# Performance work log

Hardware: AMD Instinct MI355X
Metric: run time of the kernel (lower is better)

## Reference

```python
import jax, jax.numpy as jnp
import numpy as np

D_MODEL = 1024
D_RES = 1024
EPS = 1e-5


def setup_inputs() -> dict:
    key = jax.random.key(0)
    ks = jax.random.split(key, 8)
    S, B = 2048, 32
    scale_ih = 1.0 / np.sqrt(D_MODEL)
    x = jax.random.normal(ks[0], (S, B, D_RES), dtype=jnp.float32)
    # nn.RNN params: weight_ih_l0 [H, I], weight_hh_l0 [H, H], biases [H]
    W_ih = jax.random.uniform(ks[1], (D_MODEL, D_RES), jnp.float32, -scale_ih, scale_ih)
    W_hh = jax.random.uniform(ks[2], (D_MODEL, D_MODEL), jnp.float32, -scale_ih, scale_ih)
    b_ih = jax.random.uniform(ks[3], (D_MODEL,), jnp.float32, -scale_ih, scale_ih)
    b_hh = jax.random.uniform(ks[4], (D_MODEL,), jnp.float32, -scale_ih, scale_ih)
    # out_proj: Linear(d_model, d_res, bias=False) -> weight [d_res, d_model]
    W_out = jax.random.uniform(ks[5], (D_RES, D_MODEL), jnp.float32, -scale_ih, scale_ih)
    ln_g = jnp.ones((D_RES,), jnp.float32)
    ln_b = jnp.zeros((D_RES,), jnp.float32)
    return {"x": x, "W_ih": W_ih, "W_hh": W_hh, "b_ih": b_ih, "b_hh": b_hh,
            "W_out": W_out, "ln_g": ln_g, "ln_b": ln_b}


def _layer_norm(x, g, b):
    mu = jnp.mean(x, axis=-1, keepdims=True)
    var = jnp.mean(jnp.square(x - mu), axis=-1, keepdims=True)
    return (x - mu) * jax.lax.rsqrt(var + EPS) * g + b


def _rnn_tanh(x, W_ih, W_hh, b_ih, b_hh):
    # x: [S, B, I]; precompute input projection once (one big GEMM)
    pre = jnp.einsum('sbi,hi->sbh', x, W_ih) + b_ih + b_hh  # [S, B, H]
    B = x.shape[1]
    h0 = jnp.zeros((B, W_hh.shape[0]), x.dtype)

    def step(h, p_t):
        h_new = jnp.tanh(p_t + h @ W_hh.T)
        return h_new, h_new

    _, hs = jax.lax.scan(step, h0, pre)  # hs: [S, B, H]
    return hs


def reference(x, W_ih, W_hh, b_ih, b_hh, W_out, ln_g, ln_b):
    # pre_lnorm=False, use_out_proj=True, use_res=True, use_lnorm=True, dropout=0 (eval)
    attn_out = _rnn_tanh(x, W_ih, W_hh, b_ih, b_hh)          # [S, B, d_model]
    attn_out = jnp.einsum('sbh,rh->sbr', attn_out, W_out)    # [S, B, d_res]
    return _layer_norm(x + attn_out, ln_g, ln_b)
```

## Files before the change

### kernel.cpp

```cpp
#include <hip/hip_runtime.h>
#include <hip/hip_bf16.h>

typedef __bf16 bf16x8 __attribute__((ext_vector_type(8)));
typedef __bf16 bf16x4 __attribute__((ext_vector_type(4)));
typedef float  f32x4  __attribute__((ext_vector_type(4)));
typedef unsigned int u32x2 __attribute__((ext_vector_type(2)));
typedef unsigned int u32x4 __attribute__((ext_vector_type(4)));

#define NSTEP 2048
#define NB    32
#define DH    1024
#define MTOT  (NSTEP * NB)
#define NWORK 16
#define NFILL 208
#define FILLER_CAP 60000

__device__ __forceinline__ f32x4 mfma16(bf16x8 a, bf16x8 b, f32x4 c) {
    return __builtin_amdgcn_mfma_f32_16x16x32_bf16(a, b, c, 0, 0, 0);
}

__device__ __forceinline__ void load_lds16(const __bf16* g, void* l) {
    __builtin_amdgcn_global_load_lds(
        (const __attribute__((address_space(1))) void*)g,
        (__attribute__((address_space(3))) void*)l, 16, 0, 0);
}

__device__ __forceinline__ float tanh_fast(float x) {
    float e = exp2f(x * 2.8853900817779268f);
    return 1.0f - 2.0f * __builtin_amdgcn_rcpf(e + 1.0f);
}

__global__ __launch_bounds__(256) void prep_kernel(
    const float* __restrict__ Wih, const float* __restrict__ Whh,
    const float* __restrict__ Wout, const float* __restrict__ bih,
    const float* __restrict__ bhh,
    __bf16* __restrict__ Wih_b, __bf16* __restrict__ Whh_b,
    __bf16* __restrict__ Wout_b, float* __restrict__ bias,
    int* __restrict__ flags)
{
    const int i = blockIdx.x * 256 + threadIdx.x;
    const size_t off = (size_t)i * 4;
    {
        float4 a = *(const float4*)(Wih + off);
        bf16x4 o = {(__bf16)a.x, (__bf16)a.y, (__bf16)a.z, (__bf16)a.w};
        *(bf16x4*)(Wih_b + off) = o;
    }
    {
        float4 a = *(const float4*)(Whh + off);
        bf16x4 o = {(__bf16)a.x, (__bf16)a.y, (__bf16)a.z, (__bf16)a.w};
        *(bf16x4*)(Whh_b + off) = o;
    }
    {
        float4 a = *(const float4*)(Wout + off);
        bf16x4 o = {(__bf16)a.x, (__bf16)a.y, (__bf16)a.z, (__bf16)a.w};
        *(bf16x4*)(Wout_b + off) = o;
    }
    if (i < DH) bias[i] = bih[i] + bhh[i];
    if (i < 64) {
        int z = 0;
        asm volatile("global_store_dword %0, %1, off sc0 sc1"
                     :: "v"(&flags[i]), "v"(z) : "memory");
    }
}

__global__ __launch_bounds__(256) void cvt_bf16_x(
    const float* __restrict__ in, __bf16* __restrict__ outb)
{
    const size_t i = ((size_t)blockIdx.x * 256 + threadIdx.x) * 8;
    float4 a = *(const float4*)(in + i);
    float4 b = *(const float4*)(in + i + 4);
    bf16x8 o = { (__bf16)a.x, (__bf16)a.y, (__bf16)a.z, (__bf16)a.w,
                 (__bf16)b.x, (__bf16)b.y, (__bf16)b.z, (__bf16)b.w };
    *(bf16x8*)(outb + i) = o;
}

__global__ __launch_bounds__(256) void gemm_bt(
    const __bf16* __restrict__ A,
    const __bf16* __restrict__ B,
    const float*  __restrict__ bias,
    __bf16* __restrict__ C,
    int M, int N, int K)
{
    __shared__ __bf16 sA[128 * 64];
    __shared__ __bf16 sB[128 * 64];
    const int nTn = N >> 7;
    const int tm = (int)(blockIdx.x / nTn) << 7;
    const int tn = (int)(blockIdx.x % nTn) << 7;
    const int t = threadIdx.x;
    const int w = t >> 6, l = t & 63;
    const int wy = w & 1, wx = w >> 1;
    const int l16 = l & 15, lhi = l >> 4;
    const int rw = t >> 3;
    const int kc = (t & 7) << 3;

    const __bf16* ga = A + (size_t)(tm + rw) * K + kc;
    const __bf16* gb = B + (size_t)(tn + rw) * K + kc;
    char* lA = (char*)sA + (w * 8) * 128;
    char* lB = (char*)sB + (w * 8) * 128;

    f32x4 acc[4][4] = {};

    for (int k0 = 0; k0 < K; k0 += 64) {
#pragma unroll
        for (int i = 0; i < 4; ++i) {
            load_lds16(ga + (size_t)(i * 32) * K + k0, lA + i * 32 * 128);
            load_lds16(gb + (size_t)(i * 32) * K + k0, lB + i * 32 * 128);
        }
        asm volatile("s_waitcnt vmcnt(0)" ::: "memory");
        __syncthreads();
#pragma unroll
        for (int kk = 0; kk < 2; ++kk) {
            bf16x8 af[4], bfr[4];
#pragma unroll
            for (int i = 0; i < 4; ++i) {
                af[i]  = *(const bf16x8*)(sA + (wy * 64 + i * 16 + l16) * 64 + kk * 32 + lhi * 8);
                bfr[i] = *(const bf16x8*)(sB + (wx * 64 + i * 16 + l16) * 64 + kk * 32 + lhi * 8);
            }
#pragma unroll
            for (int i = 0; i < 4; ++i)
#pragma unroll
                for (int j = 0; j < 4; ++j)
                    acc[i][j] = mfma16(af[i], bfr[j], acc[i][j]);
        }
        __syncthreads();
    }
#pragma unroll
    for (int j = 0; j < 4; ++j) {
        const int col = tn + wx * 64 + j * 16 + l16;
        const float bv = bias ? bias[col] : 0.0f;
#pragma unroll
        for (int i = 0; i < 4; ++i) {
            __bf16* cp = C + (size_t)(tm + wy * 64 + i * 16 + lhi * 4) * N + col;
#pragma unroll
            for (int r = 0; r < 4; ++r)
                cp[(size_t)r * N] = (__bf16)(acc[i][j][r] + bv);
        }
    }
}

#define LDU(d, p) asm volatile("global_load_dwordx4 %0, %1, off sc0 sc1" \
                               : "=v"(d) : "v"(p) : "memory");

__global__ __launch_bounds__(512, 2) void rnn_scan(
    const __bf16* __restrict__ Whh,
    const __bf16* __restrict__ pre,
    __bf16* __restrict__ hs,
    __bf16* __restrict__ hx,
    int* __restrict__ flags)
{
    const int gb = blockIdx.x;
    if (gb >= NWORK) {
        float a = (float)(threadIdx.x + gb) * 1.0e-6f + 1.0f;
        const float m = 1.000001f, d = 0.999999f;
        const int* dp = flags;
        for (int it = 0; it < FILLER_CAP; ++it) {
#pragma unroll
            for (int u = 0; u < 128; ++u) {
                a = __builtin_fmaf(a, m, 1.0e-12f);
                a = __builtin_fmaf(a, d, -1.0e-12f);
            }
            if ((it & 15) == 0) {
                int dn;
                asm volatile("global_load_dword %0, %1, off sc0 sc1\n\t"
                             "s_waitcnt vmcnt(0)"
                             : "=v"(dn) : "v"(dp) : "memory");
                if (dn != 0) break;
            }
        }
        asm volatile("" :: "v"(a));
        return;
    }

    __shared__ char slab[2][65536];
    const int t = threadIdx.x;
    const int w = t >> 6;
    const int l = t & 63;
    const int mhalf = w & 1;
    const int jg = w >> 1;
    const int j0 = gb * 64 + jg * 16;
    const int l16 = l & 15;
    const int lhi = l >> 4;
    const int b  = mhalf * 16 + l16;
    const int jc = j0 + lhi * 4;

    bf16x8 wreg[32];
    {
        const __bf16* wb = Whh + (size_t)(j0 + l16) * DH + lhi * 8;
#pragma unroll
        for (int c = 0; c < 32; ++c)
            wreg[c] = *(const bf16x8*)(wb + c * 32);
    }

    const unsigned rbase = (unsigned)b * 2048 + (unsigned)lhi * 16;
    const unsigned rx = (unsigned)((b & 7) << 4);

    for (int s = 0; s < NSTEP; ++s) {
        bf16x4 pv = *(const bf16x4*)(pre + ((size_t)s * NB + b) * DH + jc);

        f32x4 acc0 = {0.f, 0.f, 0.f, 0.f}, acc1 = acc0, acc2 = acc0, acc3 = acc0;
        int bi = 0;

        if (s > 0) {
            const int sl = s - 1;
            bi = sl & 1;
            const unsigned rep = (unsigned)(((sl >> 1) & 1) + 1) * 0x00010001u;
            const char* sp = (const char*)hx + ((size_t)(sl & 1) << 16) + (size_t)t * 16;
            const char* p0 = sp;
            const char* p1 = sp + 8192;
            const char* p2 = sp + 16384;
            const char* p3 = sp + 24576;
            const char* p4 = sp + 32768;
            const char* p5 = sp + 40960;
            const char* p6 = sp + 49152;
            const char* p7 = sp + 57344;
            u32x4 st[8];
            for (;;) {
                LDU(st[0], p0) LDU(st[1], p1) LDU(st[2], p2) LDU(st[3], p3)
                LDU(st[4], p4) LDU(st[5], p5) LDU(st[6], p6) LDU(st[7], p7)
                asm volatile("s_waitcnt vmcnt(0)" ::: "memory");
                __builtin_amdgcn_sched_barrier(0);
                unsigned bad = 0;
#pragma unroll
                for (int i = 0; i < 8; ++i)
                    bad |= (st[i][0] ^ rep) | (st[i][1] ^ rep)
                         | (st[i][2] ^ rep) | (st[i][3] ^ rep);
                if (__all((bad & 0x00030003u) == 0u)) break;
            }
            __builtin_amdgcn_sched_barrier(0);
#pragma unroll
            for (int i = 0; i < 8; ++i) {
                unsigned byte = (unsigned)t * 16 + (unsigned)i * 8192;
                unsigned row = byte >> 11;
                unsigned swz = byte ^ ((row & 7) << 4);
                *(u32x4*)(&slab[bi][swz]) = st[i];
            }
            __syncthreads();
#pragma unroll
            for (int c = 0; c < 32; c += 4) {
                bf16x8 h0 = *(const bf16x8*)(&slab[bi][(rbase + (unsigned)(c + 0) * 64) ^ rx]);
                bf16x8 h1 = *(const bf16x8*)(&slab[bi][(rbase + (unsigned)(c + 1) * 64) ^ rx]);
                bf16x8 h2 = *(const bf16x8*)(&slab[bi][(rbase + (unsigned)(c + 2) * 64) ^ rx]);
                bf16x8 h3 = *(const bf16x8*)(&slab[bi][(rbase + (unsigned)(c + 3) * 64) ^ rx]);
                acc0 = mfma16(wreg[c + 0], h0, acc0);
                acc1 = mfma16(wreg[c + 1], h1, acc1);
                acc2 = mfma16(wreg[c + 2], h2, acc2);
                acc3 = mfma16(wreg[c + 3], h3, acc3);
            }
        }
        f32x4 accs = (acc0 + acc1) + (acc2 + acc3);

        float h0 = tanh_fast(accs[0] + (float)pv[0]);
        float h1 = tanh_fast(accs[1] + (float)pv[1]);
        float h2 = tanh_fast(accs[2] + (float)pv[2]);
        float h3 = tanh_fast(accs[3] + (float)pv[3]);
        const unsigned tag = (unsigned)(((s >> 1) & 1) + 1);
        unsigned u0 = (unsigned)__builtin_bit_cast(unsigned short, (__bf16)h0);
        unsigned u1 = (unsigned)__builtin_bit_cast(unsigned short, (__bf16)h1);
        unsigned u2 = (unsigned)__builtin_bit_cast(unsigned short, (__bf16)h2);
        unsigned u3 = (unsigned)__builtin_bit_cast(unsigned short, (__bf16)h3);
        u0 = ((u0 + 2u) & 0xFFFCu) | tag;
        u1 = ((u1 + 2u) & 0xFFFCu) | tag;
        u2 = ((u2 + 2u) & 0xFFFCu) | tag;
        u3 = ((u3 + 2u) & 0xFFFCu) | tag;
        u32x2 uval;
        uval[0] = u0 | (u1 << 16);
        uval[1] = u2 | (u3 << 16);
        __bf16* ox = hx + ((size_t)(s & 1) * NB + b) * DH + jc;
        asm volatile("global_store_dwordx2 %0, %1, off sc0 sc1"
                     :: "v"(ox), "v"(uval) : "memory");
        *(u32x2*)(hs + ((size_t)s * NB + b) * DH + jc) = uval;
    }
    if (gb == 0 && t == 0) {
        int one = 1;
        asm volatile("global_store_dword %0, %1, off sc0 sc1"
                     :: "v"(&flags[0]), "v"(one) : "memory");
    }
}

__global__ __launch_bounds__(256) void fused_ln(
    const float* __restrict__ x,
    const __bf16* __restrict__ attn,
    const float* __restrict__ gam,
    const float* __restrict__ bet,
    float* __restrict__ out)
{
    const int row = blockIdx.x;
    const int t = threadIdx.x;
    const size_t base = (size_t)row * DH + t * 4;
    float4 xv = *(const float4*)(x + base);
    bf16x4 av = *(const bf16x4*)(attn + base);
    float v0 = xv.x + (float)av[0];
    float v1 = xv.y + (float)av[1];
    float v2 = xv.z + (float)av[2];
    float v3 = xv.w + (float)av[3];
    float s1 = v0 + v1 + v2 + v3;
    float s2 = v0 * v0 + v1 * v1 + v2 * v2 + v3 * v3;
#pragma unroll
    for (int off = 32; off > 0; off >>= 1) {
        s1 += __shfl_xor(s1, off);
        s2 += __shfl_xor(s2, off);
    }
    __shared__ float red[8];
    const int w = t >> 6, l = t & 63;
    if (l == 0) { red[w] = s1; red[4 + w] = s2; }
    __syncthreads();
    float S1 = red[0] + red[1] + red[2] + red[3];
    float S2 = red[4] + red[5] + red[6] + red[7];
    const float mu = S1 * (1.0f / 1024.0f);
    const float var = S2 * (1.0f / 1024.0f) - mu * mu;
    const float rs = rsqrtf(var + 1e-5f);
    const int c = t * 4;
    float4 gv = *(const float4*)(gam + c);
    float4 bv = *(const float4*)(bet + c);
    float4 o;
    o.x = (v0 - mu) * rs * gv.x + bv.x;
    o.y = (v1 - mu) * rs * gv.y + bv.y;
    o.z = (v2 - mu) * rs * gv.z + bv.z;
    o.w = (v3 - mu) * rs * gv.w + bv.w;
    *(float4*)(out + base) = o;
}

extern "C" void kernel_launch(void* const* d_in, const int* in_sizes, int n_in,
                              void* d_out, int out_size, void* d_ws, size_t ws_size,
                              hipStream_t stream)
{
    const float* x    = (const float*)d_in[0];
    const float* Wih  = (const float*)d_in[1];
    const float* Whh  = (const float*)d_in[2];
    const float* bih  = (const float*)d_in[3];
    const float* bhh  = (const float*)d_in[4];
    const float* Wout = (const float*)d_in[5];
    const float* lng  = (const float*)d_in[6];
    const float* lnb  = (const float*)d_in[7];
    float* out = (float*)d_out;

    char* ws = (char*)d_ws;
    const size_t BIG = (size_t)MTOT * DH * sizeof(__bf16);
    __bf16* buf0   = (__bf16*)ws;
    __bf16* pre    = (__bf16*)(ws + BIG);
    __bf16* hsbuf  = (__bf16*)(ws + 2 * BIG);
    __bf16* Wih_b  = (__bf16*)(ws + 3 * BIG);
    __bf16* Whh_b  = Wih_b + (size_t)DH * DH;
    __bf16* Wout_b = Whh_b + (size_t)DH * DH;
    float*  bias   = (float*)(Wout_b + (size_t)DH * DH);
    int*    flags  = (int*)(bias + DH);
    __bf16* hx     = (__bf16*)(ws + 3 * BIG + 8 * 1024 * 1024);

    prep_kernel<<<1024, 256, 0, stream>>>(Wih, Whh, Wout, bih, bhh,
                                          Wih_b, Whh_b, Wout_b, bias, flags);
    cvt_bf16_x<<<32768, 256, 0, stream>>>(x, buf0);
    hipMemsetAsync(hx, 0, 2 * NB * DH * sizeof(__bf16), stream);
    gemm_bt<<<4096, 256, 0, stream>>>(buf0, Wih_b, bias, pre, MTOT, DH, DH);
    rnn_scan<<<NWORK + NFILL, 512, 0, stream>>>(Whh_b, pre, hsbuf, hx, flags);
    gemm_bt<<<4096, 256, 0, stream>>>(hsbuf, Wout_b, nullptr, buf0, MTOT, DH, DH);
    fused_ln<<<65536, 256, 0, stream>>>(x, buf0, lng, lnb, out);
}
```

Baseline: 8.397 ms.

## Split batch into four independent groups and pipeline RNN scan across sub-slots

Splits the 32-wide batch into four independent 8-row groups that are processed round-robin. While one group's hidden state is being published, the next group's state and pre-activations are prefetched, so the cross-block spin-wait latency is hidden behind other groups' work. Each of 8 worker blocks now owns 128 hidden columns instead of 16 blocks owning 64, with smaller LDS slabs and more filler blocks. The trade-off is that half of each MFMA tile is wasted on the 8-row batch (only half the lanes store results) and the number of sequential synchronisation rounds is four times larger.

```diff
diff --git a/kernel.cpp b/kernel.cpp
--- a/kernel.cpp
+++ b/kernel.cpp
@@ -11,9 +11,10 @@
 #define NB    32
 #define DH    1024
 #define MTOT  (NSTEP * NB)
-#define NWORK 16
-#define NFILL 208
-#define FILLER_CAP 60000
+#define NWORK 8
+#define NFILL 240
+#define FILLER_CAP 120000
+#define TMAX  (4 * NSTEP)
 
 __device__ __forceinline__ f32x4 mfma16(bf16x8 a, bf16x8 b, f32x4 c) {
     return __builtin_amdgcn_mfma_f32_16x16x32_bf16(a, b, c, 0, 0, 0);
@@ -138,10 +139,112 @@
     }
 }
 
-#define LDU(d, p) asm volatile("global_load_dwordx4 %0, %1, off sc0 sc1" \
-                               : "=v"(d) : "v"(p) : "memory");
-
-__global__ __launch_bounds__(512, 2) void rnn_scan(
+__device__ __forceinline__ void subslot(
+    int tau, int gb, int t, int bl, int jc, bool wlane,
+    unsigned wb0, unsigned wb1, unsigned rbase, unsigned rx,
+    const bf16x8* wreg,
+    const __bf16* __restrict__ pre,
+    __bf16* __restrict__ hs,
+    __bf16* __restrict__ hx,
+    char (&slab)[2][16384],
+    u32x4& pf0, u32x4& pf1, u32x2& pvn,
+    u32x2& uv, __bf16*& px, __bf16*& ps)
+{
+    const int p_ = tau & 3;
+    const int s_ = tau >> 2;
+    const int b_ = p_ * 8 + bl;
+    const int bi = tau & 1;
+    f32x4 a0 = {0.f, 0.f, 0.f, 0.f}, a1 = a0, a2 = a0, a3 = a0;
+    bf16x4 pv;
+
+    if (s_ > 0) {
+        asm volatile("s_waitcnt vmcnt(2)" ::: "memory");
+        __builtin_amdgcn_sched_barrier(0);
+        pv = __builtin_bit_cast(bf16x4, pvn);
+        const unsigned rep = (unsigned)((((s_ - 1) >> 1) & 1) + 1) * 0x00010001u;
+        const char* pb = (const char*)hx
+            + ((size_t)((p_ << 1) + ((s_ - 1) & 1)) << 14) + (size_t)t * 32;
+        for (;;) {
+            unsigned bad = (pf0[0] ^ rep) | (pf0[1] ^ rep) | (pf0[2] ^ rep) | (pf0[3] ^ rep)
+                         | (pf1[0] ^ rep) | (pf1[1] ^ rep) | (pf1[2] ^ rep) | (pf1[3] ^ rep);
+            if (__all((bad & 0x00030003u) == 0u)) break;
+            asm volatile("global_load_dwordx4 %0, %2, off sc0 sc1\n\t"
+                         "global_load_dwordx4 %1, %2, off offset:16 sc0 sc1\n\t"
+                         "s_waitcnt vmcnt(0)"
+                         : "=v"(pf0), "=v"(pf1) : "v"(pb) : "memory");
+            __builtin_amdgcn_sched_barrier(0);
+        }
+        *(u32x4*)(&slab[bi][wb0]) = pf0;
+        *(u32x4*)(&slab[bi][wb1]) = pf1;
+    } else {
+        asm volatile("global_load_dwordx2 %0, %1, off\n\t"
+                     "s_waitcnt vmcnt(0)"
+                     : "=v"(pvn)
+                     : "v"(pre + ((size_t)s_ * NB + b_) * DH + jc) : "memory");
+        __builtin_amdgcn_sched_barrier(0);
+        pv = __builtin_bit_cast(bf16x4, pvn);
+    }
+    __syncthreads();
+
+    {
+        const int t1 = tau + 1;
+        if (t1 < TMAX) {
+            const int p1 = t1 & 3, s1 = t1 >> 2;
+            if (s1 >= 1) {
+                const char* nb = (const char*)hx
+                    + ((size_t)((p1 << 1) + ((s1 - 1) & 1)) << 14) + (size_t)t * 32;
+                asm volatile("global_load_dwordx4 %0, %2, off sc0 sc1\n\t"
+                             "global_load_dwordx4 %1, %2, off offset:16 sc0 sc1"
+                             : "=v"(pf0), "=v"(pf1) : "v"(nb) : "memory");
+                asm volatile("global_load_dwordx2 %0, %1, off"
+                             : "=v"(pvn)
+                             : "v"(pre + ((size_t)s1 * NB + (p1 * 8 + bl)) * DH + jc)
+                             : "memory");
+            }
+        }
+    }
+
+    if (s_ > 0) {
+#pragma unroll
+        for (int c = 0; c < 32; c += 4) {
+            bf16x8 h0 = *(const bf16x8*)(&slab[bi][(rbase + (unsigned)(c + 0) * 64) ^ rx]);
+            bf16x8 h1 = *(const bf16x8*)(&slab[bi][(rbase + (unsigned)(c + 1) * 64) ^ rx]);
+            bf16x8 h2 = *(const bf16x8*)(&slab[bi][(rbase + (unsigned)(c + 2) * 64) ^ rx]);
+            bf16x8 h3 = *(const bf16x8*)(&slab[bi][(rbase + (unsigned)(c + 3) * 64) ^ rx]);
+            a0 = mfma16(wreg[c + 0], h0, a0);
+            a1 = mfma16(wreg[c + 1], h1, a1);
+            a2 = mfma16(wreg[c + 2], h2, a2);
+            a3 = mfma16(wreg[c + 3], h3, a3);
+        }
+    }
+    f32x4 as = (a0 + a1) + (a2 + a3);
+
+    float h0 = tanh_fast(as[0] + (float)pv[0]);
+    float h1 = tanh_fast(as[1] + (float)pv[1]);
+    float h2 = tanh_fast(as[2] + (float)pv[2]);
+    float h3 = tanh_fast(as[3] + (float)pv[3]);
+    const unsigned tag = (unsigned)(((s_ >> 1) & 1) + 1);
+    unsigned u0 = (unsigned)__builtin_bit_cast(unsigned short, (__bf16)h0);
+    unsigned u1 = (unsigned)__builtin_bit_cast(unsigned short, (__bf16)h1);
+    unsigned u2 = (unsigned)__builtin_bit_cast(unsigned short, (__bf16)h2);
+    unsigned u3 = (unsigned)__builtin_bit_cast(unsigned short, (__bf16)h3);
+    u0 = ((u0 + 2u) & 0xFFFCu) | tag;
+    u1 = ((u1 + 2u) & 0xFFFCu) | tag;
+    u2 = ((u2 + 2u) & 0xFFFCu) | tag;
+    u3 = ((u3 + 2u) & 0xFFFCu) | tag;
+    uv[0] = u0 | (u1 << 16);
+    uv[1] = u2 | (u3 << 16);
+    px = hx + ((size_t)((p_ << 1) + (s_ & 1)) << 13) + (size_t)bl * 1024 + jc;
+    ps = hs + ((size_t)s_ * NB + b_) * DH + jc;
+    if (wlane) {
+        asm volatile("global_store_dwordx2 %0, %1, off sc0 sc1"
+                     :: "v"(px), "v"(uv) : "memory");
+        asm volatile("global_store_dwordx2 %0, %1, off"
+                     :: "v"(ps), "v"(uv) : "memory");
+    }
+}
+
+__global__ __launch_bounds__(512, 1) void rnn_scan(
     const __bf16* __restrict__ Whh,
     const __bf16* __restrict__ pre,
     __bf16* __restrict__ hs,
@@ -159,7 +262,7 @@
                 a = __builtin_fmaf(a, m, 1.0e-12f);
                 a = __builtin_fmaf(a, d, -1.0e-12f);
             }
-            if ((it & 15) == 0) {
+            if ((it & 63) == 0) {
                 int dn;
                 asm volatile("global_load_dword %0, %1, off sc0 sc1\n\t"
                              "s_waitcnt vmcnt(0)"
@@ -171,17 +274,16 @@
         return;
     }
 
-    __shared__ char slab[2][65536];
+    __shared__ char slab[2][16384];
     const int t = threadIdx.x;
     const int w = t >> 6;
     const int l = t & 63;
-    const int mhalf = w & 1;
-    const int jg = w >> 1;
-    const int j0 = gb * 64 + jg * 16;
     const int l16 = l & 15;
     const int lhi = l >> 4;
-    const int b  = mhalf * 16 + l16;
+    const int bl = l16 & 7;
+    const int j0 = gb * 128 + w * 16;
     const int jc = j0 + lhi * 4;
+    const bool wlane = (l16 < 8);
 
     bf16x8 wreg[32];
     {
@@ -191,84 +293,24 @@
             wreg[c] = *(const bf16x8*)(wb + c * 32);
     }
 
-    const unsigned rbase = (unsigned)b * 2048 + (unsigned)lhi * 16;
-    const unsigned rx = (unsigned)((b & 7) << 4);
-
-    for (int s = 0; s < NSTEP; ++s) {
-        bf16x4 pv = *(const bf16x4*)(pre + ((size_t)s * NB + b) * DH + jc);
-
-        f32x4 acc0 = {0.f, 0.f, 0.f, 0.f}, acc1 = acc0, acc2 = acc0, acc3 = acc0;
-        int bi = 0;
-
-        if (s > 0) {
-            const int sl = s - 1;
-            bi = sl & 1;
-            const unsigned rep = (unsigned)(((sl >> 1) & 1) + 1) * 0x00010001u;
-            const char* sp = (const char*)hx + ((size_t)(sl & 1) << 16) + (size_t)t * 16;
-            const char* p0 = sp;
-            const char* p1 = sp + 8192;
-            const char* p2 = sp + 16384;
-            const char* p3 = sp + 24576;
-            const char* p4 = sp + 32768;
-            const char* p5 = sp + 40960;
-            const char* p6 = sp + 49152;
-            const char* p7 = sp + 57344;
-            u32x4 st[8];
-            for (;;) {
-                LDU(st[0], p0) LDU(st[1], p1) LDU(st[2], p2) LDU(st[3], p3)
-                LDU(st[4], p4) LDU(st[5], p5) LDU(st[6], p6) LDU(st[7], p7)
-                asm volatile("s_waitcnt vmcnt(0)" ::: "memory");
-                __builtin_amdgcn_sched_barrier(0);
-                unsigned bad = 0;
-#pragma unroll
-                for (int i = 0; i < 8; ++i)
-                    bad |= (st[i][0] ^ rep) | (st[i][1] ^ rep)
-                         | (st[i][2] ^ rep) | (st[i][3] ^ rep);
-                if (__all((bad & 0x00030003u) == 0u)) break;
-            }
-            __builtin_amdgcn_sched_barrier(0);
-#pragma unroll
-            for (int i = 0; i < 8; ++i) {
-                unsigned byte = (unsigned)t * 16 + (unsigned)i * 8192;
-                unsigned row = byte >> 11;
-                unsigned swz = byte ^ ((row & 7) << 4);
-                *(u32x4*)(&slab[bi][swz]) = st[i];
-            }
-            __syncthreads();
-#pragma unroll
-            for (int c = 0; c < 32; c += 4) {
-                bf16x8 h0 = *(const bf16x8*)(&slab[bi][(rbase + (unsigned)(c + 0) * 64) ^ rx]);
-                bf16x8 h1 = *(const bf16x8*)(&slab[bi][(rbase + (unsigned)(c + 1) * 64) ^ rx]);
-                bf16x8 h2 = *(const bf16x8*)(&slab[bi][(rbase + (unsigned)(c + 2) * 64) ^ rx]);
-                bf16x8 h3 = *(const bf16x8*)(&slab[bi][(rbase + (unsigned)(c + 3) * 64) ^ rx]);
-                acc0 = mfma16(wreg[c + 0], h0, acc0);
-                acc1 = mfma16(wreg[c + 1], h1, acc1);
-                acc2 = mfma16(wreg[c + 2], h2, acc2);
-                acc3 = mfma16(wreg[c + 3], h3, acc3);
-            }
-        }
-        f32x4 accs = (acc0 + acc1) + (acc2 + acc3);
-
-        float h0 = tanh_fast(accs[0] + (float)pv[0]);
-        float h1 = tanh_fast(accs[1] + (float)pv[1]);
-        float h2 = tanh_fast(accs[2] + (float)pv[2]);
-        float h3 = tanh_fast(accs[3] + (float)pv[3]);
-        const unsigned tag = (unsigned)(((s >> 1) & 1) + 1);
-        unsigned u0 = (unsigned)__builtin_bit_cast(unsigned short, (__bf16)h0);
-        unsigned u1 = (unsigned)__builtin_bit_cast(unsigned short, (__bf16)h1);
-        unsigned u2 = (unsigned)__builtin_bit_cast(unsigned short, (__bf16)h2);
-        unsigned u3 = (unsigned)__builtin_bit_cast(unsigned short, (__bf16)h3);
-        u0 = ((u0 + 2u) & 0xFFFCu) | tag;
-        u1 = ((u1 + 2u) & 0xFFFCu) | tag;
-        u2 = ((u2 + 2u) & 0xFFFCu) | tag;
-        u3 = ((u3 + 2u) & 0xFFFCu) | tag;
-        u32x2 uval;
-        uval[0] = u0 | (u1 << 16);
-        uval[1] = u2 | (u3 << 16);
-        __bf16* ox = hx + ((size_t)(s & 1) * NB + b) * DH + jc;
-        asm volatile("global_store_dwordx2 %0, %1, off sc0 sc1"
-                     :: "v"(ox), "v"(uval) : "memory");
-        *(u32x2*)(hs + ((size_t)s * NB + b) * DH + jc) = uval;
+    const unsigned wrow = (unsigned)(t >> 6) & 7u;
+    const unsigned wb0 = ((unsigned)t * 32) ^ (wrow << 4);
+    const unsigned wb1 = ((unsigned)t * 32 + 16) ^ (wrow << 4);
+    const unsigned rbase = (unsigned)bl * 2048 + (unsigned)lhi * 16;
+    const unsigned rx = (unsigned)bl << 4;
+
+    u32x4 pf0 = {}, pf1 = {};
+    u32x2 pvn = {};
+    u32x2 uvA = {}, uvB = {};
+    __bf16 *pxA = hx, *psA = hs, *pxB = hx, *psB = hs;
+
+    for (int tau = 0; tau < TMAX; tau += 2) {
+        subslot(tau, gb, t, bl, jc, wlane, wb0, wb1, rbase, rx, wreg,
+                pre, hs, hx, slab, pf0, pf1, pvn, uvA, pxA, psA);
+        asm volatile("" :: "v"(uvB), "v"(pxB), "v"(psB));
+        subslot(tau + 1, gb, t, bl, jc, wlane, wb0, wb1, rbase, rx, wreg,
+                pre, hs, hx, slab, pf0, pf1, pvn, uvB, pxB, psB);
+        asm volatile("" :: "v"(uvA), "v"(pxA), "v"(psA));
     }
     if (gb == 0 && t == 0) {
         int one = 1;
@@ -349,7 +391,7 @@
     prep_kernel<<<1024, 256, 0, stream>>>(Wih, Whh, Wout, bih, bhh,
                                           Wih_b, Whh_b, Wout_b, bias, flags);
     cvt_bf16_x<<<32768, 256, 0, stream>>>(x, buf0);
-    hipMemsetAsync(hx, 0, 2 * NB * DH * sizeof(__bf16), stream);
+    hipMemsetAsync(hx, 0, 8 * 8 * DH * sizeof(__bf16), stream);
     gemm_bt<<<4096, 256, 0, stream>>>(buf0, Wih_b, bias, pre, MTOT, DH, DH);
     rnn_scan<<<NWORK + NFILL, 512, 0, stream>>>(Whh_b, pre, hsbuf, hx, flags);
     gemm_bt<<<4096, 256, 0, stream>>>(hsbuf, Wout_b, nullptr, buf0, MTOT, DH, DH);
```

Measured after the change: 13.04 ms. 1.55x slower.

## Halve RNN scan worker blocks, each wave computing both batch halves

Applied to the files above, without the earlier changes.

The persistent recurrent scan now uses 8 worker blocks instead of 16. Each wave owns 16 hidden units and computes both 16-row batch halves, so one set of W_hh register fragments serves twice the MFMA work. Fewer blocks take part in the per-step cross-block flag handshake, which is meant to cut synchronisation latency. In exchange each block does twice the compute per step, and the launch bound drops to one block per SM to leave room for the extra accumulators, so per-step latency may grow.

```diff
diff --git a/kernel.cpp b/kernel.cpp
--- a/kernel.cpp
+++ b/kernel.cpp
@@ -11,8 +11,8 @@
 #define NB    32
 #define DH    1024
 #define MTOT  (NSTEP * NB)
-#define NWORK 16
-#define NFILL 208
+#define NWORK 8
+#define NFILL 248
 #define FILLER_CAP 60000
 
 __device__ __forceinline__ f32x4 mfma16(bf16x8 a, bf16x8 b, f32x4 c) {
@@ -141,7 +141,7 @@
 #define LDU(d, p) asm volatile("global_load_dwordx4 %0, %1, off sc0 sc1" \
                                : "=v"(d) : "v"(p) : "memory");
 
-__global__ __launch_bounds__(512, 2) void rnn_scan(
+__global__ __launch_bounds__(512, 1) void rnn_scan(
     const __bf16* __restrict__ Whh,
     const __bf16* __restrict__ pre,
     __bf16* __restrict__ hs,
@@ -175,12 +175,11 @@
     const int t = threadIdx.x;
     const int w = t >> 6;
     const int l = t & 63;
-    const int mhalf = w & 1;
-    const int jg = w >> 1;
-    const int j0 = gb * 64 + jg * 16;
+    const int j0 = gb * 128 + w * 16;
     const int l16 = l & 15;
     const int lhi = l >> 4;
-    const int b  = mhalf * 16 + l16;
+    const int bA = l16;
+    const int bB = 16 + l16;
     const int jc = j0 + lhi * 4;
 
     bf16x8 wreg[32];
@@ -191,13 +190,16 @@
             wreg[c] = *(const bf16x8*)(wb + c * 32);
     }
 
-    const unsigned rbase = (unsigned)b * 2048 + (unsigned)lhi * 16;
-    const unsigned rx = (unsigned)((b & 7) << 4);
+    const unsigned rbA = (unsigned)bA * 2048 + (unsigned)lhi * 16;
+    const unsigned rbB = (unsigned)bB * 2048 + (unsigned)lhi * 16;
+    const unsigned rx = (unsigned)((bA & 7) << 4);
 
     for (int s = 0; s < NSTEP; ++s) {
-        bf16x4 pv = *(const bf16x4*)(pre + ((size_t)s * NB + b) * DH + jc);
-
-        f32x4 acc0 = {0.f, 0.f, 0.f, 0.f}, acc1 = acc0, acc2 = acc0, acc3 = acc0;
+        bf16x4 pvA = *(const bf16x4*)(pre + ((size_t)s * NB + bA) * DH + jc);
+        bf16x4 pvB = *(const bf16x4*)(pre + ((size_t)s * NB + bB) * DH + jc);
+
+        f32x4 aA0 = {0.f, 0.f, 0.f, 0.f}, aA1 = aA0, aA2 = aA0, aA3 = aA0;
+        f32x4 aB0 = aA0, aB1 = aA0, aB2 = aA0, aB3 = aA0;
         int bi = 0;
 
         if (s > 0) {
@@ -237,38 +239,69 @@
             __syncthreads();
 #pragma unroll
             for (int c = 0; c < 32; c += 4) {
-                bf16x8 h0 = *(const bf16x8*)(&slab[bi][(rbase + (unsigned)(c + 0) * 64) ^ rx]);
-                bf16x8 h1 = *(const bf16x8*)(&slab[bi][(rbase + (unsigned)(c + 1) * 64) ^ rx]);
-                bf16x8 h2 = *(const bf16x8*)(&slab[bi][(rbase + (unsigned)(c + 2) * 64) ^ rx]);
-                bf16x8 h3 = *(const bf16x8*)(&slab[bi][(rbase + (unsigned)(c + 3) * 64) ^ rx]);
-                acc0 = mfma16(wreg[c + 0], h0, acc0);
-                acc1 = mfma16(wreg[c + 1], h1, acc1);
-                acc2 = mfma16(wreg[c + 2], h2, acc2);
-                acc3 = mfma16(wreg[c + 3], h3, acc3);
-            }
-        }
-        f32x4 accs = (acc0 + acc1) + (acc2 + acc3);
-
-        float h0 = tanh_fast(accs[0] + (float)pv[0]);
-        float h1 = tanh_fast(accs[1] + (float)pv[1]);
-        float h2 = tanh_fast(accs[2] + (float)pv[2]);
-        float h3 = tanh_fast(accs[3] + (float)pv[3]);
+                bf16x8 hA0 = *(const bf16x8*)(&slab[bi][(rbA + (unsigned)(c + 0) * 64) ^ rx]);
+                bf16x8 hA1 = *(const bf16x8*)(&slab[bi][(rbA + (unsigned)(c + 1) * 64) ^ rx]);
+                bf16x8 hA2 = *(const bf16x8*)(&slab[bi][(rbA + (unsigned)(c + 2) * 64) ^ rx]);
+                bf16x8 hA3 = *(const bf16x8*)(&slab[bi][(rbA + (unsigned)(c + 3) * 64) ^ rx]);
+                aA0 = mfma16(wreg[c + 0], hA0, aA0);
+                aA1 = mfma16(wreg[c + 1], hA1, aA1);
+                aA2 = mfma16(wreg[c + 2], hA2, aA2);
+                aA3 = mfma16(wreg[c + 3], hA3, aA3);
+                bf16x8 hB0 = *(const bf16x8*)(&slab[bi][(rbB + (unsigned)(c + 0) * 64) ^ rx]);
+                bf16x8 hB1 = *(const bf16x8*)(&slab[bi][(rbB + (unsigned)(c + 1) * 64) ^ rx]);
+                bf16x8 hB2 = *(const bf16x8*)(&slab[bi][(rbB + (unsigned)(c + 2) * 64) ^ rx]);
+                bf16x8 hB3 = *(const bf16x8*)(&slab[bi][(rbB + (unsigned)(c + 3) * 64) ^ rx]);
+                aB0 = mfma16(wreg[c + 0], hB0, aB0);
+                aB1 = mfma16(wreg[c + 1], hB1, aB1);
+                aB2 = mfma16(wreg[c + 2], hB2, aB2);
+                aB3 = mfma16(wreg[c + 3], hB3, aB3);
+            }
+        }
+        f32x4 asA = (aA0 + aA1) + (aA2 + aA3);
+        f32x4 asB = (aB0 + aB1) + (aB2 + aB3);
+
         const unsigned tag = (unsigned)(((s >> 1) & 1) + 1);
-        unsigned u0 = (unsigned)__builtin_bit_cast(unsigned short, (__bf16)h0);
-        unsigned u1 = (unsigned)__builtin_bit_cast(unsigned short, (__bf16)h1);
-        unsigned u2 = (unsigned)__builtin_bit_cast(unsigned short, (__bf16)h2);
-        unsigned u3 = (unsigned)__builtin_bit_cast(unsigned short, (__bf16)h3);
-        u0 = ((u0 + 2u) & 0xFFFCu) | tag;
-        u1 = ((u1 + 2u) & 0xFFFCu) | tag;
-        u2 = ((u2 + 2u) & 0xFFFCu) | tag;
-        u3 = ((u3 + 2u) & 0xFFFCu) | tag;
-        u32x2 uval;
-        uval[0] = u0 | (u1 << 16);
-        uval[1] = u2 | (u3 << 16);
-        __bf16* ox = hx + ((size_t)(s & 1) * NB + b) * DH + jc;
+        u32x2 uvA, uvB;
+        {
+            float h0 = tanh_fast(asA[0] + (float)pvA[0]);
+            float h1 = tanh_fast(asA[1] + (float)pvA[1]);
+            float h2 = tanh_fast(asA[2] + (float)pvA[2]);
+            float h3 = tanh_fast(asA[3] + (float)pvA[3]);
+            unsigned u0 = (unsigned)__builtin_bit_cast(unsigned short, (__bf16)h0);
+            unsigned u1 = (unsigned)__builtin_bit_cast(unsigned short, (__bf16)h1);
+            unsigned u2 = (unsigned)__builtin_bit_cast(unsigned short, (__bf16)h2);
+            unsigned u3 = (unsigned)__builtin_bit_cast(unsigned short, (__bf16)h3);
+            u0 = ((u0 + 2u) & 0xFFFCu) | tag;
+            u1 = ((u1 + 2u) & 0xFFFCu) | tag;
+            u2 = ((u2 + 2u) & 0xFFFCu) | tag;
+            u3 = ((u3 + 2u) & 0xFFFCu) | tag;
+            uvA[0] = u0 | (u1 << 16);
+            uvA[1] = u2 | (u3 << 16);
+        }
+        {
+            float h0 = tanh_fast(asB[0] + (float)pvB[0]);
+            float h1 = tanh_fast(asB[1] + (float)pvB[1]);
+            float h2 = tanh_fast(asB[2] + (float)pvB[2]);
+            float h3 = tanh_fast(asB[3] + (float)pvB[3]);
+            unsigned u0 = (unsigned)__builtin_bit_cast(unsigned short, (__bf16)h0);
+            unsigned u1 = (unsigned)__builtin_bit_cast(unsigned short, (__bf16)h1);
+            unsigned u2 = (unsigned)__builtin_bit_cast(unsigned short, (__bf16)h2);
+            unsigned u3 = (unsigned)__builtin_bit_cast(unsigned short, (__bf16)h3);
+            u0 = ((u0 + 2u) & 0xFFFCu) | tag;
+            u1 = ((u1 + 2u) & 0xFFFCu) | tag;
+            u2 = ((u2 + 2u) & 0xFFFCu) | tag;
+            u3 = ((u3 + 2u) & 0xFFFCu) | tag;
+            uvB[0] = u0 | (u1 << 16);
+            uvB[1] = u2 | (u3 << 16);
+        }
+        __bf16* oxA = hx + ((size_t)(s & 1) * NB + bA) * DH + jc;
+        __bf16* oxB = hx + ((size_t)(s & 1) * NB + bB) * DH + jc;
         asm volatile("global_store_dwordx2 %0, %1, off sc0 sc1"
-                     :: "v"(ox), "v"(uval) : "memory");
-        *(u32x2*)(hs + ((size_t)s * NB + b) * DH + jc) = uval;
+                     :: "v"(oxA), "v"(uvA) : "memory");
+        asm volatile("global_store_dwordx2 %0, %1, off sc0 sc1"
+                     :: "v"(oxB), "v"(uvB) : "memory");
+        *(u32x2*)(hs + ((size_t)s * NB + bA) * DH + jc) = uvA;
+        *(u32x2*)(hs + ((size_t)s * NB + bB) * DH + jc) = uvB;
     }
     if (gb == 0 && t == 0) {
         int one = 1;
```

New measurement: 12.51 ms. 1.49x slower.
